# Performance work log

Measured on AMD Instinct MI355X. Metric: run time of the kernel, lower is better.

Reference implementation:

```python
import jax, jax.numpy as jnp
import numpy as np

EMBED_DIM = 512

def setup_inputs() -> dict:
    key = jax.random.key(0)
    ks = jax.random.split(key, 8)
    B, N, M, C = 4, 4096, 4096, EMBED_DIM
    s = 1.0 / np.sqrt(C)
    return {
        "rgb_features": jax.random.normal(ks[0], (B, N, C), jnp.float32),
        "depth_features": jax.random.normal(ks[1], (B, M, C), jnp.float32),
        "Wq": jax.random.normal(ks[2], (C, C), jnp.float32) * s,
        "bq": jnp.zeros((C,), jnp.float32),
        "Wk": jax.random.normal(ks[3], (C, C), jnp.float32) * s,
        "bk": jnp.zeros((C,), jnp.float32),
        "Wv": jax.random.normal(ks[4], (C, C), jnp.float32) * s,
        "bv": jnp.zeros((C,), jnp.float32),
    }

def reference(rgb_features, depth_features, Wq, bq, Wk, bk, Wv, bv):
    C = rgb_features.shape[-1]
    scale = C ** (-0.5)
    Q = rgb_features @ Wq + bq          # [B, N, C]
    K = depth_features @ Wk + bk        # [B, M, C]
    V = depth_features @ Wv + bv        # [B, M, C]
    scores = jnp.einsum('bnc,bmc->bnm', Q, K) * scale
    attn = jax.nn.softmax(scores, axis=-1)
    return jnp.einsum('bnm,bmc->bnc', attn, V)
```

## Files before the change

kernel.cpp:

```cpp
#include <hip/hip_runtime.h>
#include <hip/hip_bf16.h>
#include <stdint.h>


typedef unsigned short u16;
typedef __attribute__((ext_vector_type(8))) short bf16x8;
typedef __attribute__((ext_vector_type(16))) float f32x16;
typedef __attribute__((ext_vector_type(4))) unsigned short u16x4;

#define GLD_LDS16(g, l)                                                        \
  __builtin_amdgcn_global_load_lds(                                            \
      (const __attribute__((address_space(1))) unsigned int*)(g),              \
      (__attribute__((address_space(3))) unsigned int*)(l), 16, 0, 0)

__device__ __forceinline__ u16 f2bf(float f) {
  unsigned x = __float_as_uint(f);
  return (u16)((x + 0x7fffu + ((x >> 16) & 1u)) >> 16);
}
__device__ __forceinline__ float bf2f(short s) {
  return __uint_as_float((unsigned)(unsigned short)s << 16);
}

template <int TM, int TN, int BIAS_MODE, int OUT_MODE, int MINW>
__global__ __launch_bounds__(256, MINW) void gemm32(
    const u16* __restrict__ A, const u16* __restrict__ Bm,
    const float* __restrict__ bias, void* __restrict__ Cv, int M, int N, int K,
    long long sAb, long long sBb, long long sCb, float scale) {
  constexpr int WROWS = TM / 2;
  constexpr int WCOLS = TN / 2;
  constexpr int MSUB = WROWS / 32;
  constexpr int NSUB = WCOLS / 32;
  constexpr int CA = TM / 64;
  constexpr int CB = TN / 64;

  const int bz = blockIdx.z;
  A += (size_t)bz * sAb;
  Bm += (size_t)bz * sBb;

  const int bm = blockIdx.y * TM;
  const int bn = blockIdx.x * TN;

  __shared__ u16 As[2][TM * 32];
  __shared__ u16 Bs[2][TN * 32];

  const int tid = threadIdx.x;
  const int wave = tid >> 6;
  const int lane = tid & 63;
  const int ln31 = lane & 31;
  const int half = lane >> 5;
  const int wr = wave >> 1;
  const int wc = wave & 1;

  const int rowA = lane >> 2;
  const int swz = ((lane & 3) ^ ((rowA + (rowA >> 2)) & 3)) * 8;
  const int gl = (ln31 + (ln31 >> 2)) & 3;

  f32x16 acc[MSUB][NSUB] = {};

  auto stage = [&](int buf, int k0) {
#pragma unroll
    for (int r = 0; r < CA; ++r) {
      const int ch = wave * CA + r;
      GLD_LDS16(A + (size_t)(bm + ch * 16 + rowA) * K + k0 + swz,
                As[buf] + ch * 16 * 32);
    }
#pragma unroll
    for (int r = 0; r < CB; ++r) {
      const int ch = wave * CB + r;
      GLD_LDS16(Bm + (size_t)(bn + ch * 16 + rowA) * K + k0 + swz,
                Bs[buf] + ch * 16 * 32);
    }
  };

  const int niter = K >> 5;
  stage(0, 0);
  for (int it = 0; it < niter; ++it) {
    __syncthreads();
    if (it + 1 < niter) stage((it + 1) & 1, (it + 1) * 32);
    const int buf = it & 1;
#pragma unroll
    for (int kc = 0; kc < 2; ++kc) {
      const int p = ((kc * 2 + half) ^ gl) * 8;
      bf16x8 af[MSUB], bfv[NSUB];
#pragma unroll
      for (int mt = 0; mt < MSUB; ++mt)
        af[mt] =
            *(const bf16x8*)&As[buf][(wr * WROWS + mt * 32 + ln31) * 32 + p];
#pragma unroll
      for (int nt = 0; nt < NSUB; ++nt)
        bfv[nt] =
            *(const bf16x8*)&Bs[buf][(wc * WCOLS + nt * 32 + ln31) * 32 + p];
#pragma unroll
      for (int mt = 0; mt < MSUB; ++mt)
#pragma unroll
        for (int nt = 0; nt < NSUB; ++nt)
          acc[mt][nt] = __builtin_amdgcn_mfma_f32_32x32x16_bf16(
              af[mt], bfv[nt], acc[mt][nt], 0, 0, 0);
    }
  }

  const int crow0 = bm + wr * WROWS + 4 * half;
  const int ccol0 = bn + wc * WCOLS + ln31;
#pragma unroll
  for (int mt = 0; mt < MSUB; ++mt) {
#pragma unroll
    for (int nt = 0; nt < NSUB; ++nt) {
      const int col = ccol0 + nt * 32;
#pragma unroll
      for (int r = 0; r < 16; ++r) {
        const int row = crow0 + mt * 32 + (r & 3) + 8 * (r >> 2);
        float v = acc[mt][nt][r];
        if constexpr (BIAS_MODE == 1) v += bias[col];
        if constexpr (BIAS_MODE == 2) v += bias[row];
        const size_t idx = (size_t)bz * (size_t)sCb + (size_t)row * N + col;
        if constexpr (OUT_MODE == 0)
          ((u16*)Cv)[idx] = f2bf(v);
        else if constexpr (OUT_MODE == 1)
          ((float*)Cv)[idx] = v;
        else
          ((u16*)Cv)[idx] = f2bf(__expf(v * scale));
      }
    }
  }
}

#define XA_STGA(buf, j, k0)                                                    \
  GLD_LDS16(Ag + (size_t)((j) * 32 + (wv & 3) * 8 + (wv >> 2) * 128 + rlane) * \
                    512 +                                                      \
                (k0) + swz8,                                                   \
            &As[buf][((j) * 32 + (wv & 3) * 8 + (wv >> 2) * 128) * 64])
#define XA_STGB(buf, j, k0)                                                    \
  GLD_LDS16(Bg + (size_t)((j) * 64 + wv * 8 + rlane) * 512 + (k0) + swz8,      \
            &Bs[buf][((j) * 64 + wv * 8) * 64])

#define XA_PHASE(F, NV, PFS)                                                   \
  {                                                                            \
    bf16x8 af[4];                                                              \
    {                                                                          \
      const int arow = (wm * 128 + (F) * 32 + ln31) * 64;                      \
      _Pragma("unroll") for (int k = 0; k < 4; ++k) af[k] =                    \
          *(const bf16x8*)&As[p][arow + (((2 * k + half) ^ s7) << 3)];         \
    }                                                                          \
    if ((F) == 0) {                                                            \
      _Pragma("unroll") for (int n = 0; n < 2; ++n) {                          \
        const int brow = (wn * 64 + n * 32 + ln31) * 64;                       \
        _Pragma("unroll") for (int k = 0; k < 4; ++k) bfr[n][k] =              \
            *(const bf16x8*)&Bs[p][brow + (((2 * k + half) ^ s7) << 3)];       \
      }                                                                        \
    }                                                                          \
    PFS;                                                                       \
    __builtin_amdgcn_s_barrier();                                              \
    asm volatile("s_waitcnt lgkmcnt(0)" ::: "memory");                         \
    __builtin_amdgcn_sched_barrier(0);                                         \
    __builtin_amdgcn_s_setprio(1);                                             \
    _Pragma("unroll") for (int k = 0; k < 4; ++k) {                            \
      acc[F][0] = __builtin_amdgcn_mfma_f32_32x32x16_bf16(af[k], bfr[0][k],    \
                                                          acc[F][0], 0, 0, 0); \
      acc[F][1] = __builtin_amdgcn_mfma_f32_32x32x16_bf16(af[k], bfr[1][k],    \
                                                          acc[F][1], 0, 0, 0); \
    }                                                                          \
    __builtin_amdgcn_s_setprio(0);                                             \
    asm volatile("s_waitcnt vmcnt(" NV ")" ::: "memory");                      \
    __builtin_amdgcn_s_barrier();                                              \
    asm volatile("" ::: "memory");                                             \
  }

__global__ __launch_bounds__(512, 2) void gemm256_exp(
    const u16* __restrict__ Qm, const u16* __restrict__ Km,
    u16* __restrict__ Sout, long long sAb, long long sSb, float scale) {
  const int bz = blockIdx.z;
  const int bm = blockIdx.y * 256;
  const int bn = blockIdx.x * 256;
  const u16* Ag = Qm + (size_t)bz * (size_t)sAb + (size_t)bm * 512;
  const u16* Bg = Km + (size_t)bz * (size_t)sAb + (size_t)bn * 512;

  __shared__ u16 As[2][256 * 64];
  __shared__ u16 Bs[2][256 * 64];

  const int tid = threadIdx.x;
  const int wv = tid >> 6;
  const int lane = tid & 63;
  const int ln31 = lane & 31;
  const int half = lane >> 5;
  const int wm = wv >> 2;
  const int wn = wv & 3;
  const int rlane = lane >> 3;
  const int swz8 = ((lane & 7) ^ rlane) << 3;
  const int s7 = ln31 & 7;

  f32x16 acc[4][2] = {};
  bf16x8 bfr[2][4];

#pragma unroll
  for (int j = 0; j < 4; ++j) XA_STGB(0, j, 0);
#pragma unroll
  for (int j = 0; j < 4; ++j) XA_STGA(0, j, 0);
  asm volatile("s_waitcnt vmcnt(3)" ::: "memory");
  __builtin_amdgcn_s_barrier();
  asm volatile("" ::: "memory");

  for (int t = 0; t < 7; ++t) {
    const int p = t & 1;
    const int q = p ^ 1;
    const int kn = (t + 1) << 6;
    XA_PHASE(0, "4", { XA_STGB(q, 0, kn); XA_STGB(q, 1, kn); });
    XA_PHASE(1, "5", { XA_STGB(q, 2, kn); XA_STGB(q, 3, kn); });
    XA_PHASE(2, "6", { XA_STGA(q, 0, kn); XA_STGA(q, 1, kn); });
    XA_PHASE(3, "3", { XA_STGA(q, 2, kn); XA_STGA(q, 3, kn); });
  }
  {
    const int p = 1;
    XA_PHASE(0, "2", {});
    XA_PHASE(1, "1", {});
    XA_PHASE(2, "0", {});
    XA_PHASE(3, "0", {});
  }

  const size_t ob = (size_t)bz * (size_t)sSb;
  const int c0 = bn + wn * 64 + ln31;
  const int r0 = bm + wm * 128 + 4 * half;
#pragma unroll
  for (int m = 0; m < 4; ++m) {
#pragma unroll
    for (int n = 0; n < 2; ++n) {
      const int col = c0 + n * 32;
#pragma unroll
      for (int r = 0; r < 16; ++r) {
        const int row = r0 + m * 32 + (r & 3) + 8 * (r >> 2);
        Sout[ob + (size_t)row * 4096 + col] = f2bf(__expf(acc[m][n][r] * scale));
      }
    }
  }
}

#define PV_BODY(IT, NV, DO_STAGE, DO_TAIL)                                     \
  {                                                                            \
    const int buf = (IT) % 3;                                                  \
    if (DO_STAGE) stage(((IT) + 2) % 3, ((IT) + 2) * 64);                      \
    bf16x8 af[4][2], bfv[4][2];                                                \
    _Pragma("unroll") for (int pl = 0; pl < 2; ++pl) {                         \
      _Pragma("unroll") for (int kc = 0; kc < 2; ++kc) {                       \
        const int ks = pl * 2 + kc;                                            \
        const int p = ((kc * 2 + half) ^ gl) * 8;                              \
        _Pragma("unroll") for (int mt = 0; mt < 2; ++mt)                       \
          af[ks][mt] = *(const bf16x8*)&As[buf][(pl * 128 + wm * 64 +          \
                                                 mt * 32 + ln31) * 32 + p];    \
        _Pragma("unroll") for (int nt = 0; nt < 2; ++nt)                       \
          bfv[ks][nt] = *(const bf16x8*)&Bs[buf][(pl * 256 + wn * 64 +         \
                                                  nt * 32 + ln31) * 32 + p];   \
      }                                                                        \
    }                                                                          \
    asm volatile("s_waitcnt lgkmcnt(0)" ::: "memory");                         \
    __builtin_amdgcn_sched_barrier(0);                                         \
    __builtin_amdgcn_s_setprio(1);                                             \
    _Pragma("unroll") for (int ks = 0; ks < 4; ++ks) {                         \
      _Pragma("unroll") for (int mt = 0; mt < 2; ++mt) {                       \
        dacc[mt] = __builtin_amdgcn_mfma_f32_32x32x16_bf16(                    \
            af[ks][mt], onesv, dacc[mt], 0, 0, 0);                             \
        _Pragma("unroll") for (int nt = 0; nt < 2; ++nt)                       \
          acc[mt][nt] = __builtin_amdgcn_mfma_f32_32x32x16_bf16(               \
              af[ks][mt], bfv[ks][nt], acc[mt][nt], 0, 0, 0);                  \
      }                                                                        \
    }                                                                          \
    __builtin_amdgcn_s_setprio(0);                                             \
    if (DO_TAIL) {                                                             \
      asm volatile("s_waitcnt vmcnt(" NV ")" ::: "memory");                    \
      __builtin_amdgcn_s_barrier();                                            \
      asm volatile("" ::: "memory");                                           \
    }                                                                          \
  }

__global__ __launch_bounds__(512, 2) void pv_gemm(
    const u16* __restrict__ P, const u16* __restrict__ Vt,
    float* __restrict__ O) {
  const int bz = blockIdx.z;
  const u16* A = P + (size_t)bz * (4096ull * 4096ull);
  const u16* B = Vt + (size_t)bz * (512ull * 4096ull);
  float* Ob = O + (size_t)bz * (4096ull * 512ull);

  const int bm = blockIdx.y * 128;
  const int bn = blockIdx.x * 256;

  __shared__ u16 As[3][2 * 128 * 32];
  __shared__ u16 Bs[3][2 * 256 * 32];

  const int tid = threadIdx.x;
  const int wv = tid >> 6;
  const int lane = tid & 63;
  const int ln31 = lane & 31;
  const int half = lane >> 5;
  const int wm = wv >> 2;
  const int wn = wv & 3;

  const int rowA = lane >> 2;
  const int swz = ((lane & 3) ^ ((rowA + (rowA >> 2)) & 3)) * 8;
  const int gl = (ln31 + (ln31 >> 2)) & 3;

  f32x16 acc[2][2] = {};
  f32x16 dacc[2] = {};
  bf16x8 onesv;
#pragma unroll
  for (int j = 0; j < 8; ++j) onesv[j] = (short)0x3F80;

  auto stage = [&](int buf, int k0) {
#pragma unroll
    for (int r = 0; r < 2; ++r) {
      const int id = wv * 2 + r;
      const int pl = id >> 3, rg = id & 7;
      GLD_LDS16(A + (size_t)(bm + rg * 16 + rowA) * 4096 + k0 + pl * 32 + swz,
                As[buf] + (pl * 128 + rg * 16) * 32);
    }
#pragma unroll
    for (int r = 0; r < 4; ++r) {
      const int id = wv * 4 + r;
      const int pl = id >> 4, rg = id & 15;
      GLD_LDS16(B + (size_t)(bn + rg * 16 + rowA) * 4096 + k0 + pl * 32 + swz,
                Bs[buf] + (pl * 256 + rg * 16) * 32);
    }
  };

  stage(0, 0);
  stage(1, 64);
  asm volatile("s_waitcnt vmcnt(6)" ::: "memory");
  __builtin_amdgcn_s_barrier();
  asm volatile("" ::: "memory");

  for (int it = 0; it < 62; ++it) PV_BODY(it, "6", true, true);
  PV_BODY(62, "0", false, true);
  PV_BODY(63, "0", false, false);

  const int crow0 = bm + wm * 64 + 4 * half;
  const int ccol0 = bn + wn * 64 + ln31;
#pragma unroll
  for (int mt = 0; mt < 2; ++mt) {
#pragma unroll
    for (int r = 0; r < 16; ++r) {
      const int rl = crow0 + mt * 32 + (r & 3) + 8 * (r >> 2);
      const float rd = 1.0f / dacc[mt][r];
#pragma unroll
      for (int nt = 0; nt < 2; ++nt)
        Ob[(size_t)rl * 512 + ccol0 + nt * 32] = acc[mt][nt][r] * rd;
    }
  }
}

__global__ __launch_bounds__(256) void cvt_pair(const float* __restrict__ x,
                                                const float* __restrict__ y,
                                                u16* __restrict__ ox,
                                                u16* __restrict__ oy, int n4) {
  const int i = blockIdx.x * 256 + threadIdx.x;
  if (i >= n4) return;
  const float4 a = ((const float4*)x)[i];
  const float4 b = ((const float4*)y)[i];
  u16x4 oa, ob;
  oa[0] = f2bf(a.x); oa[1] = f2bf(a.y); oa[2] = f2bf(a.z); oa[3] = f2bf(a.w);
  ob[0] = f2bf(b.x); ob[1] = f2bf(b.y); ob[2] = f2bf(b.z); ob[3] = f2bf(b.w);
  ((u16x4*)ox)[i] = oa;
  ((u16x4*)oy)[i] = ob;
}

__global__ __launch_bounds__(256) void wtrans_k3(
    const float* __restrict__ Wq, const float* __restrict__ Wk,
    const float* __restrict__ Wv, u16* __restrict__ WqT,
    u16* __restrict__ WkT, u16* __restrict__ WvT) {
  const int z = blockIdx.z;
  const float* W = z == 0 ? Wq : (z == 1 ? Wk : Wv);
  u16* WT = z == 0 ? WqT : (z == 1 ? WkT : WvT);
  const int tr = blockIdx.y * 64;
  const int tc = blockIdx.x * 64;
  __shared__ float T[64][65];
  const int t = threadIdx.x;
  const int r0 = t >> 4;
  const int c0 = (t & 15) * 4;
#pragma unroll
  for (int rr = 0; rr < 4; ++rr) {
    const int row = rr * 16 + r0;
    const float4 w = *(const float4*)&W[(size_t)(tr + row) * 512 + tc + c0];
    T[row][c0 + 0] = w.x; T[row][c0 + 1] = w.y;
    T[row][c0 + 2] = w.z; T[row][c0 + 3] = w.w;
  }
  __syncthreads();
#pragma unroll
  for (int rr = 0; rr < 4; ++rr) {
    const int orow = rr * 16 + r0;
    u16x4 o;
#pragma unroll
    for (int j = 0; j < 4; ++j) o[j] = f2bf(T[c0 + j][orow]);
    *(u16x4*)&WT[(size_t)(tc + orow) * 512 + tr + c0] = o;
  }
}

extern "C" void kernel_launch(void* const* d_in, const int* in_sizes, int n_in,
                              void* d_out, int out_size, void* d_ws,
                              size_t ws_size, hipStream_t stream) {
  const float* rgb = (const float*)d_in[0];
  const float* dep = (const float*)d_in[1];
  const float* Wq = (const float*)d_in[2];
  const float* bq = (const float*)d_in[3];
  const float* Wk = (const float*)d_in[4];
  const float* bk = (const float*)d_in[5];
  const float* Wv = (const float*)d_in[6];
  const float* bv = (const float*)d_in[7];
  float* out = (float*)d_out;

  const int B = 4, N = 4096, M = 4096, C = 512;
  const size_t nBNC = (size_t)B * N * C;
  const float scale = 0.044194173824159216f;

  char* ws = (char*)d_ws;
  size_t off = 0;
  auto carve = [&](size_t bytes) -> void* {
    void* p = ws + off;
    off += (bytes + 255) & ~(size_t)255;
    return p;
  };
  u16* rgb_bf = (u16*)carve(nBNC * 2);
  u16* dep_bf = (u16*)carve(nBNC * 2);
  u16* WqT = (u16*)carve((size_t)C * C * 2);
  u16* WkT = (u16*)carve((size_t)C * C * 2);
  u16* WvT = (u16*)carve((size_t)C * C * 2);
  u16* Qb = (u16*)carve(nBNC * 2);
  u16* Kb = (u16*)carve(nBNC * 2);
  u16* Vt = (u16*)carve(nBNC * 2);
  u16* Sb = (u16*)carve((size_t)B * N * M * 2);

  const long long strQ = (long long)N * C;
  const long long strS = (long long)N * M;
  const long long strV = (long long)C * M;

  cvt_pair<<<8192, 256, 0, stream>>>(rgb, dep, rgb_bf, dep_bf, (int)(nBNC / 4));
  wtrans_k3<<<dim3(8, 8, 3), 256, 0, stream>>>(Wq, Wk, Wv, WqT, WkT, WvT);

  gemm32<128, 128, 1, 0, 4><<<dim3(4, 128, 1), 256, 0, stream>>>(
      rgb_bf, WqT, bq, Qb, 16384, 512, 512, 0, 0, 0, 1.f);
  gemm32<128, 128, 1, 0, 4><<<dim3(4, 128, 1), 256, 0, stream>>>(
      dep_bf, WkT, bk, Kb, 16384, 512, 512, 0, 0, 0, 1.f);
  gemm32<128, 128, 2, 0, 4><<<dim3(32, 4, 4), 256, 0, stream>>>(
      WvT, dep_bf, bv, Vt, 512, 4096, 512, 0, strQ, strV, 1.f);

  gemm256_exp<<<dim3(16, 16, 4), 512, 0, stream>>>(Qb, Kb, Sb, strQ, strS,
                                                   scale);

  pv_gemm<<<dim3(2, 32, 4), 512, 0, stream>>>(Sb, Vt, out);
}
```

Measured before the change: 365.3 us.

## Interleave LDS reads with MFMAs and split row-sum MFMAs across warps

The PV GEMM inner loop now issues shared-memory fragment reads per k-slice, interleaved with the MFMAs of the previous slice, instead of reading all fragments and waiting before computing. The row-sum (denominator) MFMA against a ones vector is now done by only one of the four column warps per k-slice, so each warp holds a partial sum. The partial sums are combined through LDS after the main loop. This cuts redundant denominator MFMAs and hides LDS latency, at the cost of an extra barrier, an LDS reduction and reliance on compiler-inserted waitcnts.

```diff
diff --git a/kernel.cpp b/kernel.cpp
--- a/kernel.cpp
+++ b/kernel.cpp
@@ -233,36 +233,51 @@
   }
 }
 
+#define PV_READ_KS(KS, BUF)                                                    \
+  {                                                                            \
+    constexpr int pl_ = (KS) >> 1;                                             \
+    constexpr int kc_ = (KS) & 1;                                              \
+    const int p = ((kc_ * 2 + half) ^ gl) * 8;                                 \
+    af[KS][0] =                                                                \
+        *(const bf16x8*)&As[BUF][(pl_ * 128 + wm * 64 + ln31) * 32 + p];       \
+    af[KS][1] =                                                                \
+        *(const bf16x8*)&As[BUF][(pl_ * 128 + wm * 64 + 32 + ln31) * 32 + p];  \
+    bfv[KS][0] =                                                               \
+        *(const bf16x8*)&Bs[BUF][(pl_ * 256 + wn * 64 + ln31) * 32 + p];       \
+    bfv[KS][1] =                                                               \
+        *(const bf16x8*)&Bs[BUF][(pl_ * 256 + wn * 64 + 32 + ln31) * 32 + p];  \
+  }
+
+#define PV_MFMA_KS(KS)                                                         \
+  {                                                                            \
+    if (wn == (KS)) {                                                          \
+      dacc[0] = __builtin_amdgcn_mfma_f32_32x32x16_bf16(af[KS][0], onesv,      \
+                                                        dacc[0], 0, 0, 0);     \
+      dacc[1] = __builtin_amdgcn_mfma_f32_32x32x16_bf16(af[KS][1], onesv,      \
+                                                        dacc[1], 0, 0, 0);     \
+    }                                                                          \
+    _Pragma("unroll") for (int mt = 0; mt < 2; ++mt)                           \
+        _Pragma("unroll") for (int nt = 0; nt < 2; ++nt) acc[mt][nt] =         \
+        __builtin_amdgcn_mfma_f32_32x32x16_bf16(af[KS][mt], bfv[KS][nt],       \
+                                                acc[mt][nt], 0, 0, 0);         \
+  }
+
 #define PV_BODY(IT, NV, DO_STAGE, DO_TAIL)                                     \
   {                                                                            \
     const int buf = (IT) % 3;                                                  \
     if (DO_STAGE) stage(((IT) + 2) % 3, ((IT) + 2) * 64);                      \
     bf16x8 af[4][2], bfv[4][2];                                                \
-    _Pragma("unroll") for (int pl = 0; pl < 2; ++pl) {                         \
-      _Pragma("unroll") for (int kc = 0; kc < 2; ++kc) {                       \
-        const int ks = pl * 2 + kc;                                            \
-        const int p = ((kc * 2 + half) ^ gl) * 8;                              \
-        _Pragma("unroll") for (int mt = 0; mt < 2; ++mt)                       \
-          af[ks][mt] = *(const bf16x8*)&As[buf][(pl * 128 + wm * 64 +          \
-                                                 mt * 32 + ln31) * 32 + p];    \
-        _Pragma("unroll") for (int nt = 0; nt < 2; ++nt)                       \
-          bfv[ks][nt] = *(const bf16x8*)&Bs[buf][(pl * 256 + wn * 64 +         \
-                                                  nt * 32 + ln31) * 32 + p];   \
-      }                                                                        \
-    }                                                                          \
-    asm volatile("s_waitcnt lgkmcnt(0)" ::: "memory");                         \
-    __builtin_amdgcn_sched_barrier(0);                                         \
     __builtin_amdgcn_s_setprio(1);                                             \
-    _Pragma("unroll") for (int ks = 0; ks < 4; ++ks) {                         \
-      _Pragma("unroll") for (int mt = 0; mt < 2; ++mt) {                       \
-        dacc[mt] = __builtin_amdgcn_mfma_f32_32x32x16_bf16(                    \
-            af[ks][mt], onesv, dacc[mt], 0, 0, 0);                             \
-        _Pragma("unroll") for (int nt = 0; nt < 2; ++nt)                       \
-          acc[mt][nt] = __builtin_amdgcn_mfma_f32_32x32x16_bf16(               \
-              af[ks][mt], bfv[ks][nt], acc[mt][nt], 0, 0, 0);                  \
-      }                                                                        \
-    }                                                                          \
+    PV_READ_KS(0, buf)                                                         \
+    PV_READ_KS(1, buf)                                                         \
+    PV_MFMA_KS(0)                                                              \
+    PV_READ_KS(2, buf)                                                         \
+    PV_MFMA_KS(1)                                                              \
+    PV_READ_KS(3, buf)                                                         \
+    PV_MFMA_KS(2)                                                              \
+    PV_MFMA_KS(3)                                                              \
     __builtin_amdgcn_s_setprio(0);                                             \
+    asm volatile("s_waitcnt lgkmcnt(0)" ::: "memory");          \
     if (DO_TAIL) {                                                             \
       asm volatile("s_waitcnt vmcnt(" NV ")" ::: "memory");                    \
       __builtin_amdgcn_s_barrier();                                            \
@@ -329,6 +344,29 @@
   PV_BODY(62, "0", false, true);
   PV_BODY(63, "0", false, false);
 
+  __builtin_amdgcn_s_barrier();
+  asm volatile("" ::: "memory");
+  float* dsum = (float*)&Bs[0][0];
+  {
+    const int base = (wv * 64 + lane) * 36;
+#pragma unroll
+    for (int mt = 0; mt < 2; ++mt)
+#pragma unroll
+      for (int r = 0; r < 16; ++r) dsum[base + mt * 16 + r] = dacc[mt][r];
+  }
+  __syncthreads();
+  float den[2][16];
+#pragma unroll
+  for (int mt = 0; mt < 2; ++mt)
+#pragma unroll
+    for (int r = 0; r < 16; ++r) {
+      float s = 0.f;
+#pragma unroll
+      for (int w = 0; w < 4; ++w)
+        s += dsum[((wm * 4 + w) * 64 + lane) * 36 + mt * 16 + r];
+      den[mt][r] = s;
+    }
+
   const int crow0 = bm + wm * 64 + 4 * half;
   const int ccol0 = bn + wn * 64 + ln31;
 #pragma unroll
@@ -336,7 +374,7 @@
 #pragma unroll
     for (int r = 0; r < 16; ++r) {
       const int rl = crow0 + mt * 32 + (r & 3) + 8 * (r >> 2);
-      const float rd = 1.0f / dacc[mt][r];
+      const float rd = 1.0f / den[mt][r];
 #pragma unroll
       for (int nt = 0; nt < 2; ++nt)
         Ob[(size_t)rl * 512 + ccol0 + nt * 32] = acc[mt][nt][r] * rd;
```

Measured after the change: 357.5 us. 1.02x faster.
